# Performance work log

Hardware: AMD Instinct MI355X
Metric: run time of the kernel (lower is better)

The kernel has to match this reference:

```python
import jax, jax.numpy as jnp
import numpy as np

EPS = 1e-12  # layer_norm_eps

def _ln(h, g, b):
    m = jnp.mean(h, axis=-1, keepdims=True)
    v = jnp.var(h, axis=-1, keepdims=True)
    return (h - m) / jnp.sqrt(v + EPS) * g + b

def setup_inputs() -> dict:
    key = jax.random.key(0)
    B, L, C, N = 32, 512, 256, 16
    ks = jax.random.split(key, 8)
    f = jax.random.normal
    return {
        'query': f(ks[0], (B, L, C), jnp.float32),
        'x': f(ks[1], (B, L, C), jnp.float32),
        'offset': f(ks[2], (B, L, 2 * N), jnp.float32) * 0.1,
        'w1': f(ks[3], (L, L // 4), jnp.float32) * 0.02, 'b1': jnp.zeros((L // 4,), jnp.float32),
        'g1': jnp.ones((L // 4,), jnp.float32), 'bt1': jnp.zeros((L // 4,), jnp.float32),
        'w2': f(ks[4], (L // 4, L), jnp.float32) * 0.02, 'b2': jnp.zeros((L,), jnp.float32),
        'w3': f(ks[5], (C, C), jnp.float32) * 0.02, 'b3': jnp.zeros((C,), jnp.float32),
        'g3': jnp.ones((C,), jnp.float32), 'bt3': jnp.zeros((C,), jnp.float32),
        'w4': f(ks[6], (C, 2 * N), jnp.float32) * 0.02, 'b4': jnp.zeros((2 * N,), jnp.float32),
    }

def reference(query, x, offset, w1, b1, g1, bt1, w2, b2, w3, b3, g3, bt3, w4, b4):
    B, L, C = x.shape
    N = w4.shape[1] // 2
    # sample_layer: Linear over the sequence axis (query permuted to [B,C,L])
    q = jnp.swapaxes(query, 1, 2)                                        # [B,C,L]
    q = jax.nn.gelu(_ln(q @ w1 + b1, g1, bt1), approximate=False) @ w2 + b2
    q = jnp.swapaxes(q, 1, 2)                                            # [B,L,C]
    # adjust_layer over channels -> per-step 2N offsets, tanh * 0.02
    adj = jax.nn.gelu(_ln(q @ w3 + b3, g3, bt3), approximate=False) @ w4 + b4
    adj = jnp.tanh(adj) * 0.02                                           # [B,L,2N]
    local = (offset + adj).reshape(B, L, N, 2)
    # precomputed reference points (x-coord 0, y-coord depends on query step i)
    i = jnp.arange(L, dtype=x.dtype)
    n = jnp.arange(N, dtype=x.dtype) + 0.5
    ref_y = n[None, :] * 2.0 * (i[:, None] + 1e-9) / (N * L) - 1.0       # [L,N]
    ref = jnp.stack([jnp.zeros_like(ref_y), ref_y], axis=-1)             # [L,N,2]
    pos = jnp.tanh(local + ref[None])                                    # [B,L,N,2]
    # grid_sample equivalent: input [B*L, C, H=L, W=1], align_corners=True,
    # bilinear, zero padding. With W=1 the x-coordinate always maps to col 0,
    # so only pos[...,1] matters. Causal mask zeroes keys h > query step l
    # before sampling; since bilinear sampling is linear in the input, we mask
    # the two gathered taps instead of materializing the O(B*L*L*C) tensor.
    pix = (pos[..., 1] + 1.0) * 0.5 * (L - 1)                            # [B,L,N]
    i0f = jnp.floor(pix)
    frac = pix - i0f
    i0 = i0f.astype(jnp.int32)
    i1 = i0 + 1
    lpos = jnp.arange(L, dtype=jnp.int32)[None, :, None]
    v0 = (i0 >= 0) & (i0 < L) & (i0 <= lpos)
    v1 = (i1 >= 0) & (i1 < L) & (i1 <= lpos)
    c0 = jnp.clip(i0, 0, L - 1)
    c1 = jnp.clip(i1, 0, L - 1)
    bidx = jnp.arange(B)[:, None, None]
    val0 = x[bidx, c0]                                                   # [B,L,N,C]
    val1 = x[bidx, c1]                                                   # [B,L,N,C]
    w0 = jnp.where(v0, 1.0 - frac, 0.0)
    w1_ = jnp.where(v1, frac, 0.0)
    out = w0[..., None] * val0 + w1_[..., None] * val1                   # [B,L,N,C]
    return (out, offset, pos)
```

## Files before the change

### kernel.cpp

```cpp
#include <hip/hip_runtime.h>
#include <hip/hip_fp16.h>
#include <math.h>


typedef _Float16 f16;
typedef _Float16 f16x8 __attribute__((ext_vector_type(8)));
typedef float f32x4 __attribute__((ext_vector_type(4)));

#define ZERO4 f32x4{0.f, 0.f, 0.f, 0.f}

__device__ __forceinline__ float gelu_exact(float v) {
  return 0.5f * v * (1.0f + erff(v * 0.70710678118654752f));
}

__global__ __launch_bounds__(256) void k0_prep(
    const float* __restrict__ w1, const float* __restrict__ w2,
    const float* __restrict__ w3, const float* __restrict__ w4,
    f16* __restrict__ w1T, f16* __restrict__ w2T,
    f16* __restrict__ w3T, f16* __restrict__ w4T) {
  __shared__ f16 tile[64][80];
  int blk = blockIdx.x;
  const float* in; f16* out; int R, Cc, tr, tc;
  if (blk < 16)      { in = w1; out = w1T; R = 512; Cc = 128; tr = blk >> 1; tc = blk & 1; }
  else if (blk < 32) { blk -= 16; in = w2; out = w2T; R = 128; Cc = 512; tr = blk >> 3; tc = blk & 7; }
  else if (blk < 48) { blk -= 32; in = w3; out = w3T; R = 256; Cc = 256; tr = blk >> 2; tc = blk & 3; }
  else               { blk -= 48; in = w4; out = w4T; R = 256; Cc = 32;  tr = blk;      tc = 0; }
  const int r0 = tr * 64, c0 = tc * 64;
  const int tid = threadIdx.x;
  for (int id = tid; id < 4096; id += 256) {
    int rr = id >> 6, cc = id & 63;
    if (c0 + cc < Cc) tile[cc][rr] = (f16)in[(r0 + rr) * Cc + c0 + cc];
  }
  __syncthreads();
  for (int id = tid; id < 512; id += 256) {
    int cc = id >> 3, ch = id & 7;
    if (c0 + cc < Cc)
      *(f16x8*)(out + (c0 + cc) * R + r0 + ch * 8) = *(f16x8*)&tile[cc][ch * 8];
  }
}

__global__ __launch_bounds__(256) void k1_gemm1(
    const float* __restrict__ query, const f16* __restrict__ w1T,
    const float* __restrict__ b1, const float* __restrict__ g1,
    const float* __restrict__ bt1, f16* __restrict__ t1) {
  __shared__ char At[16 * 128];
  __shared__ char Bt[128 * 128];
  __shared__ float hs[16][132];
  const int tid = threadIdx.x;
  const int b = blockIdx.x >> 4;
  const int c0 = (blockIdx.x & 15) << 4;
  const int lane = tid & 63, w = tid >> 6;
  const int mrow = lane & 15, kg = lane >> 4;

  f32x4 acc[2] = {ZERO4, ZERO4};
  for (int s = 0; s < 8; ++s) {
    const int k0 = s << 6;
    for (int id = tid; id < 1024; id += 256) {
      int k = id >> 4, r = id & 15;
      float v = query[((b << 9) + k0 + k) * 256 + c0 + r];
      *(f16*)(At + r * 128 + ((k << 1) ^ ((r & 7) << 4))) = (f16)v;
    }
    for (int id = tid; id < 1024; id += 256) {
      int rj = id >> 3, c = id & 7;
      f16x8 v = *(const f16x8*)(w1T + rj * 512 + k0 + c * 8);
      *(f16x8*)(Bt + rj * 128 + ((c * 16) ^ ((rj & 7) << 4))) = v;
    }
    __syncthreads();
#pragma unroll
    for (int kk = 0; kk < 2; ++kk) {
      f16x8 a = *(const f16x8*)(At + mrow * 128 + (((kk << 6) + (kg << 4)) ^ ((mrow & 7) << 4)));
#pragma unroll
      for (int nf = 0; nf < 2; ++nf) {
        int rn = w * 32 + nf * 16 + mrow;
        f16x8 bfr = *(const f16x8*)(Bt + rn * 128 + (((kk << 6) + (kg << 4)) ^ ((rn & 7) << 4)));
        acc[nf] = __builtin_amdgcn_mfma_f32_16x16x32_f16(a, bfr, acc[nf], 0, 0, 0);
      }
    }
    __syncthreads();
  }
#pragma unroll
  for (int nf = 0; nf < 2; ++nf)
#pragma unroll
    for (int i = 0; i < 4; ++i)
      hs[kg * 4 + i][w * 32 + nf * 16 + mrow] = acc[nf][i];
  __syncthreads();
  const int r = tid >> 4, g = tid & 15;
  float s1 = 0.f, s2 = 0.f, vals[8];
#pragma unroll
  for (int jj = 0; jj < 8; ++jj) {
    int j = g * 8 + jj;
    float v = hs[r][j] + b1[j];
    vals[jj] = v; s1 += v; s2 += v * v;
  }
#pragma unroll
  for (int m = 1; m < 16; m <<= 1) { s1 += __shfl_xor(s1, m, 64); s2 += __shfl_xor(s2, m, 64); }
  const float mean = s1 * (1.f / 128.f);
  float var = fmaxf(s2 * (1.f / 128.f) - mean * mean, 0.f);
  const float rstd = rsqrtf(var + 1e-12f);
  f16 ov[8];
#pragma unroll
  for (int jj = 0; jj < 8; ++jj) {
    int j = g * 8 + jj;
    float v = (vals[jj] - mean) * rstd * g1[j] + bt1[j];
    ov[jj] = (f16)gelu_exact(v);
  }
  *(f16x8*)(t1 + ((b << 8) + c0 + r) * 128 + g * 8) = *(f16x8*)ov;
}

__global__ __launch_bounds__(256) void k2_gemm2(
    const f16* __restrict__ w2T, const f16* __restrict__ t1,
    const float* __restrict__ b2, f16* __restrict__ qout) {
  __shared__ char At[64 * 128];
  __shared__ char Bt[64 * 128];
  const int tid = threadIdx.x;
  const int b = blockIdx.x >> 5;
  const int l0 = ((blockIdx.x >> 2) & 7) << 6;
  const int c0 = (blockIdx.x & 3) << 6;
  const int lane = tid & 63, w = tid >> 6;
  const int mh = w >> 1, nh = w & 1;
  const int mrow = lane & 15, kg = lane >> 4;

  f32x4 acc[2][2] = {{ZERO4, ZERO4}, {ZERO4, ZERO4}};
  for (int s = 0; s < 2; ++s) {
    const int k0 = s << 6;
    for (int id = tid; id < 512; id += 256) {
      int r = id >> 3, c = id & 7;
      f16x8 v = *(const f16x8*)(w2T + (l0 + r) * 128 + k0 + c * 8);
      *(f16x8*)(At + r * 128 + ((c * 16) ^ ((r & 7) << 4))) = v;
    }
    for (int id = tid; id < 512; id += 256) {
      int r = id >> 3, c = id & 7;
      f16x8 v = *(const f16x8*)(t1 + ((b << 8) + c0 + r) * 128 + k0 + c * 8);
      *(f16x8*)(Bt + r * 128 + ((c * 16) ^ ((r & 7) << 4))) = v;
    }
    __syncthreads();
#pragma unroll
    for (int kk = 0; kk < 2; ++kk) {
      f16x8 a[2], bb[2];
#pragma unroll
      for (int mf = 0; mf < 2; ++mf) {
        int rm = mh * 32 + mf * 16 + mrow;
        a[mf] = *(const f16x8*)(At + rm * 128 + (((kk << 6) + (kg << 4)) ^ ((rm & 7) << 4)));
      }
#pragma unroll
      for (int nf = 0; nf < 2; ++nf) {
        int rn = nh * 32 + nf * 16 + mrow;
        bb[nf] = *(const f16x8*)(Bt + rn * 128 + (((kk << 6) + (kg << 4)) ^ ((rn & 7) << 4)));
      }
#pragma unroll
      for (int mf = 0; mf < 2; ++mf)
#pragma unroll
        for (int nf = 0; nf < 2; ++nf)
          acc[mf][nf] = __builtin_amdgcn_mfma_f32_16x16x32_f16(a[mf], bb[nf], acc[mf][nf], 0, 0, 0);
    }
    __syncthreads();
  }
#pragma unroll
  for (int mf = 0; mf < 2; ++mf) {
#pragma unroll
    for (int i = 0; i < 4; ++i) {
      int l = l0 + mh * 32 + mf * 16 + kg * 4 + i;
      float bb2 = b2[l];
#pragma unroll
      for (int nf = 0; nf < 2; ++nf)
        qout[((b << 9) + l) * 256 + c0 + nh * 32 + nf * 16 + mrow] = (f16)(acc[mf][nf][i] + bb2);
    }
  }
}

__global__ __launch_bounds__(256) void k3_adjust(
    const f16* __restrict__ qbuf, const f16* __restrict__ w3T,
    const float* __restrict__ b3, const float* __restrict__ g3,
    const float* __restrict__ bt3, const f16* __restrict__ w4T,
    const float* __restrict__ b4, const float* __restrict__ offset,
    float* __restrict__ off_out, float* __restrict__ pos_out) {
  __shared__ char pool[50176];
  __shared__ char w4t[32 * 512];
  __shared__ float sb3[256];
  const int tid = threadIdx.x;
  const int b = blockIdx.x >> 4;
  const int l0 = (blockIdx.x & 15) << 5;
  const int lane = tid & 63, w = tid >> 6;
  const int mh = w & 1, nh = w >> 1;
  const int mrow = lane & 15, kg = lane >> 4;
  char* At = pool;
  char* Bt = pool + 4096;

  for (int id = tid; id < 1024; id += 256) {
    int r = id >> 5, c = id & 31;
    f16x8 v = *(const f16x8*)(w4T + r * 256 + c * 8);
    *(f16x8*)(w4t + r * 512 + ((c * 16) ^ ((r & 7) << 4))) = v;
  }
  sb3[tid] = b3[tid];

  f32x4 acc[8] = {ZERO4, ZERO4, ZERO4, ZERO4, ZERO4, ZERO4, ZERO4, ZERO4};
  for (int s = 0; s < 4; ++s) {
    const int k0 = s << 6;
    {
      int r = tid >> 3, c = tid & 7;
      f16x8 v = *(const f16x8*)(qbuf + ((b << 9) + l0 + r) * 256 + k0 + c * 8);
      *(f16x8*)(At + r * 128 + ((c * 16) ^ ((r & 7) << 4))) = v;
    }
    for (int id = tid; id < 2048; id += 256) {
      int r = id >> 3, c = id & 7;
      f16x8 v = *(const f16x8*)(w3T + r * 256 + k0 + c * 8);
      *(f16x8*)(Bt + r * 128 + ((c * 16) ^ ((r & 7) << 4))) = v;
    }
    __syncthreads();
#pragma unroll
    for (int kk = 0; kk < 2; ++kk) {
      int arow = mh * 16 + mrow;
      f16x8 a = *(const f16x8*)(At + arow * 128 + (((kk << 6) + (kg << 4)) ^ ((arow & 7) << 4)));
#pragma unroll
      for (int nf = 0; nf < 8; ++nf) {
        int rn = nh * 128 + nf * 16 + mrow;
        f16x8 bfr = *(const f16x8*)(Bt + rn * 128 + (((kk << 6) + (kg << 4)) ^ ((rn & 7) << 4)));
        acc[nf] = __builtin_amdgcn_mfma_f32_16x16x32_f16(a, bfr, acc[nf], 0, 0, 0);
      }
    }
    __syncthreads();
  }
  float (*hs)[264] = (float(*)[264])pool;
  char* ts = pool + 33792;
#pragma unroll
  for (int nf = 0; nf < 8; ++nf) {
    int col = nh * 128 + nf * 16 + mrow;
    float bias = sb3[col];
#pragma unroll
    for (int i = 0; i < 4; ++i)
      hs[mh * 16 + kg * 4 + i][col] = acc[nf][i] + bias;
  }
  __syncthreads();
  for (int p = 0; p < 2; ++p) {
    const int r = p * 16 + (tid >> 4), g = tid & 15;
    float s1 = 0.f, s2 = 0.f, vals[16];
#pragma unroll
    for (int jj = 0; jj < 16; ++jj) {
      float v = hs[r][g * 16 + jj];
      vals[jj] = v; s1 += v; s2 += v * v;
    }
#pragma unroll
    for (int m = 1; m < 16; m <<= 1) { s1 += __shfl_xor(s1, m, 64); s2 += __shfl_xor(s2, m, 64); }
    const float mean = s1 * (1.f / 256.f);
    float var = fmaxf(s2 * (1.f / 256.f) - mean * mean, 0.f);
    const float rstd = rsqrtf(var + 1e-12f);
    f16 ov[16];
#pragma unroll
    for (int jj = 0; jj < 16; ++jj) {
      int kch = g * 16 + jj;
      float v = (vals[jj] - mean) * rstd * g3[kch] + bt3[kch];
      ov[jj] = (f16)gelu_exact(v);
    }
    *(f16x8*)(ts + r * 512 + ((g * 32) ^ ((r & 7) << 4))) = *(f16x8*)&ov[0];
    *(f16x8*)(ts + r * 512 + ((g * 32 + 16) ^ ((r & 7) << 4))) = *(f16x8*)&ov[8];
  }
  __syncthreads();
  const int mf = w & 1, n4 = w >> 1;
  f32x4 a4 = ZERO4;
#pragma unroll
  for (int ks = 0; ks < 8; ++ks) {
    int ar = mf * 16 + mrow;
    f16x8 a = *(const f16x8*)(ts + ar * 512 + (((ks << 6) + (kg << 4)) ^ ((ar & 7) << 4)));
    int br = n4 * 16 + mrow;
    f16x8 bb = *(const f16x8*)(w4t + br * 512 + (((ks << 6) + (kg << 4)) ^ ((br & 7) << 4)));
    a4 = __builtin_amdgcn_mfma_f32_16x16x32_f16(a, bb, a4, 0, 0, 0);
  }
  const int col = n4 * 16 + mrow;
#pragma unroll
  for (int i = 0; i < 4; ++i) {
    const int row = mf * 16 + kg * 4 + i;
    const int l = l0 + row;
    float adj = tanhf(a4[i] + b4[col]) * 0.02f;
    float padj = __shfl_xor(adj, 1, 64);
    if ((lane & 1) == 0) {
      const int n = col >> 1;
      const float2 offv = *(const float2*)(offset + (((b << 9) + l) << 5) + col);
      const float pos0v = tanhf(offv.x + adj);
      const float ref_y = ((float)n + 0.5f) * ((float)l + 1e-9f) * (1.0f / 4096.0f) - 1.0f;
      const float pos1v = tanhf(offv.y + padj + ref_y);
      *(float2*)(off_out + (((b << 9) + l) << 5) + col) = offv;
      *(float2*)(pos_out + (((b << 9) + l) << 5) + col) = make_float2(pos0v, pos1v);
    }
  }
}

__global__ __launch_bounds__(256) void k4_gather(
    const float* __restrict__ x, const float* __restrict__ pos,
    float* __restrict__ outbuf) {
  const unsigned u = blockIdx.x * 256u + threadIdx.x;
  const unsigned t_idx = u >> 6;
  const unsigned cj = u & 63;
  const int b = t_idx >> 13;
  const int l = (t_idx >> 4) & 511;
  const float pos1 = pos[t_idx * 2 + 1];
  const float pix = (pos1 + 1.0f) * 0.5f * 511.0f;
  const float i0f = floorf(pix);
  const int i0 = (int)i0f;
  const float frac = pix - i0f;
  const int i1 = i0 + 1;
  const bool v0 = (i0 >= 0) && (i0 < 512) && (i0 <= l);
  const bool v1 = (i1 >= 0) && (i1 < 512) && (i1 <= l);
  const int c0 = i0 < 0 ? 0 : (i0 > 511 ? 511 : i0);
  const int c1 = i1 < 0 ? 0 : (i1 > 511 ? 511 : i1);
  const float w0  = v0 ? (1.0f - frac) : 0.0f;
  const float w1v = v1 ? frac : 0.0f;
  const float4* x4 = (const float4*)x;
  const float4 va = x4[(unsigned)((b << 9) + c0) * 64u + cj];
  const float4 vb = x4[(unsigned)((b << 9) + c1) * 64u + cj];
  float4 o;
  o.x = w0 * va.x + w1v * vb.x;
  o.y = w0 * va.y + w1v * vb.y;
  o.z = w0 * va.z + w1v * vb.z;
  o.w = w0 * va.w + w1v * vb.w;
  ((float4*)outbuf)[u] = o;
}

extern "C" void kernel_launch(void* const* d_in, const int* in_sizes, int n_in,
                              void* d_out, int out_size, void* d_ws, size_t ws_size,
                              hipStream_t stream) {
  const float* query  = (const float*)d_in[0];
  const float* x      = (const float*)d_in[1];
  const float* offset = (const float*)d_in[2];
  const float* w1  = (const float*)d_in[3];
  const float* b1  = (const float*)d_in[4];
  const float* g1  = (const float*)d_in[5];
  const float* bt1 = (const float*)d_in[6];
  const float* w2  = (const float*)d_in[7];
  const float* b2  = (const float*)d_in[8];
  const float* w3  = (const float*)d_in[9];
  const float* b3  = (const float*)d_in[10];
  const float* g3  = (const float*)d_in[11];
  const float* bt3 = (const float*)d_in[12];
  const float* w4  = (const float*)d_in[13];
  const float* b4  = (const float*)d_in[14];

  float* out     = (float*)d_out;
  float* off_out = out + 67108864;
  float* pos_out = off_out + 524288;

  f16* wsbase = (f16*)d_ws;
  f16* w1T = wsbase;
  f16* w2T = w1T + 65536;
  f16* w3T = w2T + 65536;
  f16* w4T = w3T + 65536;
  f16* t1  = w4T + 8192;
  f16* q   = t1 + 1048576;

  k0_prep<<<52, 256, 0, stream>>>(w1, w2, w3, w4, w1T, w2T, w3T, w4T);
  k1_gemm1<<<512, 256, 0, stream>>>(query, w1T, b1, g1, bt1, t1);
  k2_gemm2<<<1024, 256, 0, stream>>>(w2T, t1, b2, q);
  k3_adjust<<<512, 256, 0, stream>>>(q, w3T, b3, g3, bt3, w4T, b4, offset,
                                     off_out, pos_out);
  k4_gather<<<65536, 256, 0, stream>>>(x, pos_out, out);
}
```

Measured before the change: 121.8 us.

## Fuse sample-layer GEMMs into one kernel and pre-transpose query to f16

The two sample-layer GEMMs are merged into one kernel, so the LayerNorm+GELU intermediate t1 stays in shared memory instead of round-tripping through global memory. The query transpose and f16 conversion move into the prep kernel, letting the first GEMM load contiguous f16x8 vectors instead of strided scalar floats. In exchange, the prep kernel now writes a full transposed query copy, and each fused block reloads all of w2T and writes q with narrow 16-column stores.

New measurement: 122.4 us. No clear change (+0.4%).

```diff
diff --git a/kernel.cpp b/kernel.cpp
--- a/kernel.cpp
+++ b/kernel.cpp
@@ -16,49 +16,72 @@
 __global__ __launch_bounds__(256) void k0_prep(
     const float* __restrict__ w1, const float* __restrict__ w2,
     const float* __restrict__ w3, const float* __restrict__ w4,
+    const float* __restrict__ query,
     f16* __restrict__ w1T, f16* __restrict__ w2T,
-    f16* __restrict__ w3T, f16* __restrict__ w4T) {
+    f16* __restrict__ w3T, f16* __restrict__ w4T, f16* __restrict__ qT) {
   __shared__ f16 tile[64][80];
   int blk = blockIdx.x;
-  const float* in; f16* out; int R, Cc, tr, tc;
-  if (blk < 16)      { in = w1; out = w1T; R = 512; Cc = 128; tr = blk >> 1; tc = blk & 1; }
-  else if (blk < 32) { blk -= 16; in = w2; out = w2T; R = 128; Cc = 512; tr = blk >> 3; tc = blk & 7; }
-  else if (blk < 48) { blk -= 32; in = w3; out = w3T; R = 256; Cc = 256; tr = blk >> 2; tc = blk & 3; }
-  else               { blk -= 48; in = w4; out = w4T; R = 256; Cc = 32;  tr = blk;      tc = 0; }
-  const int r0 = tr * 64, c0 = tc * 64;
   const int tid = threadIdx.x;
-  for (int id = tid; id < 4096; id += 256) {
-    int rr = id >> 6, cc = id & 63;
-    if (c0 + cc < Cc) tile[cc][rr] = (f16)in[(r0 + rr) * Cc + c0 + cc];
-  }
-  __syncthreads();
-  for (int id = tid; id < 512; id += 256) {
-    int cc = id >> 3, ch = id & 7;
-    if (c0 + cc < Cc)
-      *(f16x8*)(out + (c0 + cc) * R + r0 + ch * 8) = *(f16x8*)&tile[cc][ch * 8];
-  }
-}
-
-__global__ __launch_bounds__(256) void k1_gemm1(
-    const float* __restrict__ query, const f16* __restrict__ w1T,
+  if (blk < 52) {
+    const float* in; f16* out; int R, Cc, tr, tc;
+    if (blk < 16)      { in = w1; out = w1T; R = 512; Cc = 128; tr = blk >> 1; tc = blk & 1; }
+    else if (blk < 32) { blk -= 16; in = w2; out = w2T; R = 128; Cc = 512; tr = blk >> 3; tc = blk & 7; }
+    else if (blk < 48) { blk -= 32; in = w3; out = w3T; R = 256; Cc = 256; tr = blk >> 2; tc = blk & 3; }
+    else               { blk -= 48; in = w4; out = w4T; R = 256; Cc = 32;  tr = blk;      tc = 0; }
+    const int r0 = tr * 64, c0 = tc * 64;
+    for (int id = tid; id < 4096; id += 256) {
+      int rr = id >> 6, cc = id & 63;
+      if (c0 + cc < Cc) tile[cc][rr] = (f16)in[(r0 + rr) * Cc + c0 + cc];
+    }
+    __syncthreads();
+    for (int id = tid; id < 512; id += 256) {
+      int cc = id >> 3, ch = id & 7;
+      if (c0 + cc < Cc)
+        *(f16x8*)(out + (c0 + cc) * R + r0 + ch * 8) = *(f16x8*)&tile[cc][ch * 8];
+    }
+  } else {
+    blk -= 52;
+    const int b = blk >> 5, t = blk & 31;
+    const int l0 = (t >> 2) << 6, c0 = (t & 3) << 6;
+    for (int id = tid; id < 4096; id += 256) {
+      int rr = id >> 6, cc = id & 63;
+      tile[cc][rr] = (f16)query[((b << 9) + l0 + rr) * 256 + c0 + cc];
+    }
+    __syncthreads();
+    for (int id = tid; id < 512; id += 256) {
+      int cc = id >> 3, ch = id & 7;
+      *(f16x8*)(qT + ((b << 8) + c0 + cc) * 512 + l0 + ch * 8) = *(f16x8*)&tile[cc][ch * 8];
+    }
+  }
+}
+
+__global__ __launch_bounds__(256) void k12_sample(
+    const f16* __restrict__ qT, const f16* __restrict__ w1T,
+    const f16* __restrict__ w2T,
     const float* __restrict__ b1, const float* __restrict__ g1,
-    const float* __restrict__ bt1, f16* __restrict__ t1) {
-  __shared__ char At[16 * 128];
-  __shared__ char Bt[128 * 128];
-  __shared__ float hs[16][132];
+    const float* __restrict__ bt1, const float* __restrict__ b2,
+    f16* __restrict__ qout) {
+  __shared__ char pool[38912];
   const int tid = threadIdx.x;
   const int b = blockIdx.x >> 4;
   const int c0 = (blockIdx.x & 15) << 4;
   const int lane = tid & 63, w = tid >> 6;
   const int mrow = lane & 15, kg = lane >> 4;
+  char* At = pool;
+  char* Bt = pool + 2048;
+  char* t1s = pool + 32768;
+  float* sb2 = (float*)(pool + 36864);
+
+  sb2[tid] = b2[tid];
+  sb2[tid + 256] = b2[tid + 256];
 
   f32x4 acc[2] = {ZERO4, ZERO4};
   for (int s = 0; s < 8; ++s) {
     const int k0 = s << 6;
-    for (int id = tid; id < 1024; id += 256) {
-      int k = id >> 4, r = id & 15;
-      float v = query[((b << 9) + k0 + k) * 256 + c0 + r];
-      *(f16*)(At + r * 128 + ((k << 1) ^ ((r & 7) << 4))) = (f16)v;
+    if (tid < 128) {
+      int r = tid >> 3, c = tid & 7;
+      f16x8 v = *(const f16x8*)(qT + ((b << 8) + c0 + r) * 512 + k0 + c * 8);
+      *(f16x8*)(At + r * 128 + ((c * 16) ^ ((r & 7) << 4))) = v;
     }
     for (int id = tid; id < 1024; id += 256) {
       int rj = id >> 3, c = id & 7;
@@ -78,93 +101,66 @@
     }
     __syncthreads();
   }
+  float (*hs)[132] = (float(*)[132])pool;
 #pragma unroll
   for (int nf = 0; nf < 2; ++nf)
 #pragma unroll
     for (int i = 0; i < 4; ++i)
       hs[kg * 4 + i][w * 32 + nf * 16 + mrow] = acc[nf][i];
   __syncthreads();
-  const int r = tid >> 4, g = tid & 15;
-  float s1 = 0.f, s2 = 0.f, vals[8];
-#pragma unroll
-  for (int jj = 0; jj < 8; ++jj) {
-    int j = g * 8 + jj;
-    float v = hs[r][j] + b1[j];
-    vals[jj] = v; s1 += v; s2 += v * v;
-  }
-#pragma unroll
-  for (int m = 1; m < 16; m <<= 1) { s1 += __shfl_xor(s1, m, 64); s2 += __shfl_xor(s2, m, 64); }
-  const float mean = s1 * (1.f / 128.f);
-  float var = fmaxf(s2 * (1.f / 128.f) - mean * mean, 0.f);
-  const float rstd = rsqrtf(var + 1e-12f);
-  f16 ov[8];
-#pragma unroll
-  for (int jj = 0; jj < 8; ++jj) {
-    int j = g * 8 + jj;
-    float v = (vals[jj] - mean) * rstd * g1[j] + bt1[j];
-    ov[jj] = (f16)gelu_exact(v);
-  }
-  *(f16x8*)(t1 + ((b << 8) + c0 + r) * 128 + g * 8) = *(f16x8*)ov;
-}
-
-__global__ __launch_bounds__(256) void k2_gemm2(
-    const f16* __restrict__ w2T, const f16* __restrict__ t1,
-    const float* __restrict__ b2, f16* __restrict__ qout) {
-  __shared__ char At[64 * 128];
-  __shared__ char Bt[64 * 128];
-  const int tid = threadIdx.x;
-  const int b = blockIdx.x >> 5;
-  const int l0 = ((blockIdx.x >> 2) & 7) << 6;
-  const int c0 = (blockIdx.x & 3) << 6;
-  const int lane = tid & 63, w = tid >> 6;
-  const int mh = w >> 1, nh = w & 1;
-  const int mrow = lane & 15, kg = lane >> 4;
-
-  f32x4 acc[2][2] = {{ZERO4, ZERO4}, {ZERO4, ZERO4}};
-  for (int s = 0; s < 2; ++s) {
-    const int k0 = s << 6;
-    for (int id = tid; id < 512; id += 256) {
-      int r = id >> 3, c = id & 7;
-      f16x8 v = *(const f16x8*)(w2T + (l0 + r) * 128 + k0 + c * 8);
-      *(f16x8*)(At + r * 128 + ((c * 16) ^ ((r & 7) << 4))) = v;
-    }
-    for (int id = tid; id < 512; id += 256) {
-      int r = id >> 3, c = id & 7;
-      f16x8 v = *(const f16x8*)(t1 + ((b << 8) + c0 + r) * 128 + k0 + c * 8);
-      *(f16x8*)(Bt + r * 128 + ((c * 16) ^ ((r & 7) << 4))) = v;
-    }
-    __syncthreads();
-#pragma unroll
-    for (int kk = 0; kk < 2; ++kk) {
-      f16x8 a[2], bb[2];
+  {
+    const int r = tid >> 4, g = tid & 15;
+    float s1 = 0.f, s2 = 0.f, vals[8];
+#pragma unroll
+    for (int jj = 0; jj < 8; ++jj) {
+      int j = g * 8 + jj;
+      float v = hs[r][j] + b1[j];
+      vals[jj] = v; s1 += v; s2 += v * v;
+    }
+#pragma unroll
+    for (int m = 1; m < 16; m <<= 1) { s1 += __shfl_xor(s1, m, 64); s2 += __shfl_xor(s2, m, 64); }
+    const float mean = s1 * (1.f / 128.f);
+    float var = fmaxf(s2 * (1.f / 128.f) - mean * mean, 0.f);
+    const float rstd = rsqrtf(var + 1e-12f);
+    f16 ov[8];
+#pragma unroll
+    for (int jj = 0; jj < 8; ++jj) {
+      int j = g * 8 + jj;
+      float v = (vals[jj] - mean) * rstd * g1[j] + bt1[j];
+      ov[jj] = (f16)gelu_exact(v);
+    }
+    __syncthreads();
+    *(f16x8*)(t1s + r * 256 + ((g * 16) ^ ((r & 7) << 4))) = *(f16x8*)ov;
+  }
+  __syncthreads();
+
+  char* At2 = pool;
+  for (int lc = 0; lc < 4; ++lc) {
+    for (int id = tid; id < 2048; id += 256) {
+      int r = id >> 4, c = id & 15;
+      f16x8 v = *(const f16x8*)(w2T + (lc * 128 + r) * 128 + c * 8);
+      *(f16x8*)(At2 + r * 256 + ((c * 16) ^ ((r & 7) << 4))) = v;
+    }
+    __syncthreads();
+    f32x4 acc2[2] = {ZERO4, ZERO4};
+#pragma unroll
+    for (int ks = 0; ks < 4; ++ks) {
+      f16x8 bfr = *(const f16x8*)(t1s + mrow * 256 + (((ks << 6) + (kg << 4)) ^ ((mrow & 7) << 4)));
 #pragma unroll
       for (int mf = 0; mf < 2; ++mf) {
-        int rm = mh * 32 + mf * 16 + mrow;
-        a[mf] = *(const f16x8*)(At + rm * 128 + (((kk << 6) + (kg << 4)) ^ ((rm & 7) << 4)));
+        int rm = w * 32 + mf * 16 + mrow;
+        f16x8 a = *(const f16x8*)(At2 + rm * 256 + (((ks << 6) + (kg << 4)) ^ ((rm & 7) << 4)));
+        acc2[mf] = __builtin_amdgcn_mfma_f32_16x16x32_f16(a, bfr, acc2[mf], 0, 0, 0);
       }
-#pragma unroll
-      for (int nf = 0; nf < 2; ++nf) {
-        int rn = nh * 32 + nf * 16 + mrow;
-        bb[nf] = *(const f16x8*)(Bt + rn * 128 + (((kk << 6) + (kg << 4)) ^ ((rn & 7) << 4)));
+    }
+#pragma unroll
+    for (int mf = 0; mf < 2; ++mf)
+#pragma unroll
+      for (int i = 0; i < 4; ++i) {
+        int l = lc * 128 + w * 32 + mf * 16 + kg * 4 + i;
+        qout[((b << 9) + l) * 256 + c0 + mrow] = (f16)(acc2[mf][i] + sb2[l]);
       }
-#pragma unroll
-      for (int mf = 0; mf < 2; ++mf)
-#pragma unroll
-        for (int nf = 0; nf < 2; ++nf)
-          acc[mf][nf] = __builtin_amdgcn_mfma_f32_16x16x32_f16(a[mf], bb[nf], acc[mf][nf], 0, 0, 0);
-    }
-    __syncthreads();
-  }
-#pragma unroll
-  for (int mf = 0; mf < 2; ++mf) {
-#pragma unroll
-    for (int i = 0; i < 4; ++i) {
-      int l = l0 + mh * 32 + mf * 16 + kg * 4 + i;
-      float bb2 = b2[l];
-#pragma unroll
-      for (int nf = 0; nf < 2; ++nf)
-        qout[((b << 9) + l) * 256 + c0 + nh * 32 + nf * 16 + mrow] = (f16)(acc[mf][nf][i] + bb2);
-    }
+    __syncthreads();
   }
 }
 
@@ -338,17 +334,15 @@
   float* off_out = out + 67108864;
   float* pos_out = off_out + 524288;
 
-  f16* wsbase = (f16*)d_ws;
-  f16* w1T = wsbase;
+  f16* w1T = (f16*)d_ws;
   f16* w2T = w1T + 65536;
   f16* w3T = w2T + 65536;
   f16* w4T = w3T + 65536;
-  f16* t1  = w4T + 8192;
-  f16* q   = t1 + 1048576;
-
-  k0_prep<<<52, 256, 0, stream>>>(w1, w2, w3, w4, w1T, w2T, w3T, w4T);
-  k1_gemm1<<<512, 256, 0, stream>>>(query, w1T, b1, g1, bt1, t1);
-  k2_gemm2<<<1024, 256, 0, stream>>>(w2T, t1, b2, q);
+  f16* qT  = w4T + 8192;
+  f16* q   = qT + 4194304;
+
+  k0_prep<<<1076, 256, 0, stream>>>(w1, w2, w3, w4, query, w1T, w2T, w3T, w4T, qT);
+  k12_sample<<<512, 256, 0, stream>>>(qT, w1T, w2T, b1, g1, bt1, b2, q);
   k3_adjust<<<512, 256, 0, stream>>>(q, w3T, b3, g3, bt3, w4T, b4, offset,
                                      off_out, pos_out);
   k4_gather<<<65536, 256, 0, stream>>>(x, pos_out, out);
```
